# Kernel tuning notes

Hardware: AMD Instinct MI355X
Metric: run time of the kernel (lower is better)

Reference implementation:

```python
import jax, jax.numpy as jnp
import numpy as np

H = 16      # num_heads
D = 64      # head_dim
BQ = 64     # block_size_q
BKV = 64    # block_size_kv


def setup_inputs() -> dict:
    key = jax.random.key(0)
    ks = jax.random.split(key, 5)
    B, S, dim = 2, 2048, 1024
    x = jax.random.normal(ks[0], (B, S, dim), dtype=jnp.float32)
    Wq = jax.random.normal(ks[1], (dim, H * D), dtype=jnp.float32) * 0.02
    Wk = jax.random.normal(ks[2], (dim, H * D), dtype=jnp.float32) * 0.02
    Wv = jax.random.normal(ks[3], (dim, H * D), dtype=jnp.float32) * 0.02
    Wo = jax.random.normal(ks[4], (H * D, dim), dtype=jnp.float32) * 0.02
    return {"x": x, "Wq": Wq, "Wk": Wk, "Wv": Wv, "Wo": Wo}


def _flash_tiled(q, k, v, scale):
    # q,k,v: (B, H, S, D). Non-causal tiled attention with online softmax,
    # faithfully replicating the source's per-iteration division by l_new.
    B, nh, S, d = q.shape
    nq, nkv = S // BQ, S // BKV
    qb = q.reshape(B, nh, nq, BQ, d)                       # all q blocks at once (outer loop vectorized)
    kb = k.reshape(B, nh, nkv, BKV, d).transpose(2, 0, 1, 3, 4)  # (nkv, B, H, BKV, D)
    vb = v.reshape(B, nh, nkv, BKV, d).transpose(2, 0, 1, 3, 4)

    o0 = jnp.zeros((B, nh, nq, BQ, d), q.dtype)
    m0 = jnp.full((B, nh, nq, BQ), -jnp.inf, q.dtype)
    l0 = jnp.zeros((B, nh, nq, BQ), q.dtype)

    def step(carry, kv):
        o, m, l = carry
        kj, vj = kv
        s = jnp.einsum('bhnqd,bhkd->bhnqk', qb, kj) * scale   # (B,H,nq,BQ,BKV)
        m_new = jnp.maximum(m, s.max(axis=-1))
        p = jnp.exp(s - m_new[..., None])
        alpha = jnp.exp(m - m_new)
        l_new = alpha * l + p.sum(axis=-1)
        # NOTE: division by l_new every iteration, as in the source module.
        o_new = (alpha[..., None] * o + jnp.einsum('bhnqk,bhkd->bhnqd', p, vj)) / l_new[..., None]
        return (o_new, m_new, l_new), None

    (o, _, _), _ = jax.lax.scan(step, (o0, m0, l0), (kb, vb))
    return o.reshape(B, nh, S, d)


def reference(x, Wq, Wk, Wv, Wo):
    B, S, dim = x.shape
    scale = D ** -0.5
    q = (x @ Wq).reshape(B, S, H, D).transpose(0, 2, 1, 3)
    k = (x @ Wk).reshape(B, S, H, D).transpose(0, 2, 1, 3)
    v = (x @ Wv).reshape(B, S, H, D).transpose(0, 2, 1, 3)
    o = _flash_tiled(q, k, v, scale)                       # (B,H,S,D)
    out = o.transpose(0, 2, 1, 3).reshape(B, S, H * D)
    return out @ Wo
```

## Files before the change

### kernel.cpp

```cpp
#include <hip/hip_runtime.h>
#include <hip/hip_bf16.h>
#include <math.h>

#define BB   2
#define SS   2048
#define DIM  1024
#define NH   16
#define HD   64
#define MTOT (BB * SS)

typedef unsigned short ushortT;
typedef __attribute__((ext_vector_type(8))) short short8v;
typedef __attribute__((ext_vector_type(4))) float float4v;

union FragU { short8v v; unsigned short us[8]; unsigned int u[4]; };

__device__ inline unsigned short f2bf(float x) {
    unsigned u = __builtin_bit_cast(unsigned, x);
    u += 0x7fffu + ((u >> 16) & 1u);
    return (unsigned short)(u >> 16);
}
__device__ inline float bf2f(unsigned short h) {
    unsigned u = ((unsigned)h) << 16;
    return __builtin_bit_cast(float, u);
}
__device__ inline void split_tr(float x, unsigned short& hi, unsigned short& lo) {
    unsigned u = __builtin_bit_cast(unsigned, x);
    hi = (unsigned short)(u >> 16);
    float hf = __builtin_bit_cast(float, u & 0xffff0000u);
    lo = (unsigned short)(__builtin_bit_cast(unsigned, x - hf) >> 16);
}
__device__ inline void split4(const float4& x, short4& hi, short4& lo) {
    unsigned short h0 = f2bf(x.x), h1 = f2bf(x.y), h2 = f2bf(x.z), h3 = f2bf(x.w);
    hi = make_short4((short)h0, (short)h1, (short)h2, (short)h3);
    lo = make_short4((short)f2bf(x.x - bf2f(h0)), (short)f2bf(x.y - bf2f(h1)),
                     (short)f2bf(x.z - bf2f(h2)), (short)f2bf(x.w - bf2f(h3)));
}
__device__ inline void gld_lds16(const void* g, void* l) {
    __builtin_amdgcn_global_load_lds(
        (const __attribute__((address_space(1))) void*)g,
        (__attribute__((address_space(3))) void*)l, 16, 0, 0);
}

__global__ __launch_bounds__(256) void convert_split_kernel(
    const float* __restrict__ in, ushortT* __restrict__ hi, ushortT* __restrict__ lo, int n4)
{
    int t = blockIdx.x * 256 + threadIdx.x;
    if (t < n4) {
        float4 x = ((const float4*)in)[t];
        short4 h, l; split4(x, h, l);
        ((short4*)hi)[t] = h;
        ((short4*)lo)[t] = l;
    }
}

__global__ __launch_bounds__(256) void transpose_split_kernel(
    const float* __restrict__ W0, const float* __restrict__ W1,
    const float* __restrict__ W2, const float* __restrict__ W3,
    ushortT* __restrict__ WtH, ushortT* __restrict__ WtL)
{
    const int z = blockIdx.z;
    const float* __restrict__ W = (z == 0) ? W0 : (z == 1) ? W1 : (z == 2) ? W2 : W3;
    ushortT* H = WtH + (size_t)z * 1024 * 1024;
    ushortT* L = WtL + (size_t)z * 1024 * 1024;

    __shared__ float T[64][65];
    const int k0 = blockIdx.y * 64, n0 = blockIdx.x * 64;
    const int tid = threadIdx.x;
    const int c4 = (tid & 15) * 4;

#pragma unroll
    for (int i = 0; i < 4; i++) {
        int r = (tid >> 4) + 16 * i;
        *(float4*)&T[r][c4] = *(const float4*)(W + (size_t)(k0 + r) * 1024 + n0 + c4);
    }
    __syncthreads();
#pragma unroll
    for (int i = 0; i < 4; i++) {
        int n = (tid >> 4) + 16 * i;
        float4 vv = make_float4(T[c4 + 0][n], T[c4 + 1][n], T[c4 + 2][n], T[c4 + 3][n]);
        short4 h, l; split4(vv, h, l);
        *(short4*)&H[(size_t)(n0 + n) * 1024 + k0 + c4] = h;
        *(short4*)&L[(size_t)(n0 + n) * 1024 + k0 + c4] = l;
    }
}

__global__ __launch_bounds__(256) void kv_convert_kernel(
    const float* __restrict__ kw, const float* __restrict__ vw,
    ushortT* __restrict__ KhG, ushortT* __restrict__ KlG,
    ushortT* __restrict__ VhG, ushortT* __restrict__ VlG)
{
    const int which = blockIdx.z;
    const int jb = blockIdx.x, bh = blockIdx.y;
    const int b = bh >> 4, h = bh & 15;
    const float* __restrict__ in = which ? vw : kw;
    ushortT* __restrict__ OH = which ? VhG : KhG;
    ushortT* __restrict__ OL = which ? VlG : KlG;

    __shared__ float T[64][68];
    const int tid = threadIdx.x;
    const size_t ibase = (size_t)b * SS * DIM + (size_t)h * HD + (size_t)(jb * 64) * DIM;
    const int c4 = (tid & 15) * 4;
#pragma unroll
    for (int i = 0; i < 4; i++) {
        int r = (tid >> 4) + 16 * i;
        *(float4*)&T[r][c4] = *(const float4*)(in + ibase + (size_t)r * DIM + c4);
    }
    __syncthreads();

    ushortT* oh = OH + (size_t)(bh * 32 + jb) * 4096;
    ushortT* ol = OL + (size_t)(bh * 32 + jb) * 4096;

#pragma unroll
    for (int i = 0; i < 2; i++) {
        const int s = tid + i * 256;
        const int f = s >> 6;
        const int lane = s & 63;
        const int ks = f >> 2, c = f & 3;
        const int qd = lane >> 4, l15 = lane & 15;
        ushortT hv[8], lv[8];
        if (which == 0) {
            const int kv = c * 16 + l15;
            const int d0 = ks * 32 + qd * 8;
#pragma unroll
            for (int j = 0; j < 8; j++) split_tr(T[kv][d0 + j], hv[j], lv[j]);
        } else {
            const int d = c * 16 + l15;
            const int kv0 = ks * 32 + qd * 8;
#pragma unroll
            for (int j = 0; j < 8; j++) split_tr(T[kv0 + j][d], hv[j], lv[j]);
        }
        *(short4*)&oh[s * 8]     = *(short4*)&hv[0];
        *(short4*)&oh[s * 8 + 4] = *(short4*)&hv[4];
        *(short4*)&ol[s * 8]     = *(short4*)&lv[0];
        *(short4*)&ol[s * 8 + 4] = *(short4*)&lv[4];
    }
}

__global__ __launch_bounds__(256, 2) void gemm_bt_split_kernel(
    const ushortT* __restrict__ Ah, const ushortT* __restrict__ Al,
    const ushortT* __restrict__ BtH, const ushortT* __restrict__ BtL,
    float* __restrict__ Y0, float* __restrict__ Y1, float* __restrict__ Y2)
{
    const int z = blockIdx.z;
    const ushortT* __restrict__ Bh = BtH + (size_t)z * 1024 * 1024;
    const ushortT* __restrict__ Bl = BtL + (size_t)z * 1024 * 1024;
    float* __restrict__ Y = (z == 0) ? Y0 : (z == 1) ? Y1 : Y2;

    const int K = 1024, N = 1024;
    const int m0 = blockIdx.y * 128;
    const int n0 = blockIdx.x * 128;

    __shared__ __align__(16) ushortT AhS[128 * 32];
    __shared__ __align__(16) ushortT AlS[128 * 32];
    __shared__ __align__(16) ushortT BhS[128 * 32];
    __shared__ __align__(16) ushortT BlS[128 * 32];

    const int tid  = threadIdx.x;
    const int wave = tid >> 6, lane = tid & 63;
    const int quad = lane >> 4, l15 = lane & 15;
    const int wm = wave >> 1, wn = wave & 1;

    const int s0 = tid, s1 = tid + 256;
    const int ar0 = s0 >> 2, ak0 = (s0 & 3) * 8;
    const int ar1 = s1 >> 2, ak1 = (s1 & 3) * 8;

    float4v acc[4][4];
#pragma unroll
    for (int i = 0; i < 4; i++)
#pragma unroll
        for (int j = 0; j < 4; j++) acc[i][j] = (float4v){0.f, 0.f, 0.f, 0.f};

    for (int k0 = 0; k0 < K; k0 += 32) {
        __syncthreads();
        gld_lds16(Ah + (size_t)(m0 + ar0) * K + k0 + ak0, &AhS[s0 * 8]);
        gld_lds16(Ah + (size_t)(m0 + ar1) * K + k0 + ak1, &AhS[s1 * 8]);
        gld_lds16(Al + (size_t)(m0 + ar0) * K + k0 + ak0, &AlS[s0 * 8]);
        gld_lds16(Al + (size_t)(m0 + ar1) * K + k0 + ak1, &AlS[s1 * 8]);
        gld_lds16(Bh + (size_t)(n0 + ar0) * K + k0 + ak0, &BhS[s0 * 8]);
        gld_lds16(Bh + (size_t)(n0 + ar1) * K + k0 + ak1, &BhS[s1 * 8]);
        gld_lds16(Bl + (size_t)(n0 + ar0) * K + k0 + ak0, &BlS[s0 * 8]);
        gld_lds16(Bl + (size_t)(n0 + ar1) * K + k0 + ak1, &BlS[s1 * 8]);
        __syncthreads();

        FragU ah[4], al[4], bh[4], bl[4];
#pragma unroll
        for (int t = 0; t < 4; t++) {
            ah[t].v = *(const short8v*)&AhS[(wm * 64 + t * 16 + l15) * 32 + quad * 8];
            al[t].v = *(const short8v*)&AlS[(wm * 64 + t * 16 + l15) * 32 + quad * 8];
            bh[t].v = *(const short8v*)&BhS[(wn * 64 + t * 16 + l15) * 32 + quad * 8];
            bl[t].v = *(const short8v*)&BlS[(wn * 64 + t * 16 + l15) * 32 + quad * 8];
        }
#pragma unroll
        for (int mt = 0; mt < 4; mt++)
#pragma unroll
            for (int nt = 0; nt < 4; nt++) {
                acc[mt][nt] = __builtin_amdgcn_mfma_f32_16x16x32_bf16(ah[mt].v, bh[nt].v, acc[mt][nt], 0, 0, 0);
                acc[mt][nt] = __builtin_amdgcn_mfma_f32_16x16x32_bf16(ah[mt].v, bl[nt].v, acc[mt][nt], 0, 0, 0);
                acc[mt][nt] = __builtin_amdgcn_mfma_f32_16x16x32_bf16(al[mt].v, bh[nt].v, acc[mt][nt], 0, 0, 0);
            }
    }

#pragma unroll
    for (int mt = 0; mt < 4; mt++)
#pragma unroll
        for (int r = 0; r < 4; r++) {
            const int row = m0 + wm * 64 + mt * 16 + quad * 4 + r;
            float* yp = Y + (size_t)row * N + n0 + wn * 64 + l15;
#pragma unroll
            for (int nt = 0; nt < 4; nt++)
                yp[nt * 16] = acc[mt][nt][r];
        }
}

__global__ __launch_bounds__(256, 2) void attn_mfma_kernel(
    const float* __restrict__ q,
    const ushortT* __restrict__ KhG, const ushortT* __restrict__ KlG,
    const ushortT* __restrict__ VhG, const ushortT* __restrict__ VlG,
    ushortT* __restrict__ Oh, ushortT* __restrict__ Ol)
{
    __shared__ __align__(16) ushortT KhS[4096];
    __shared__ __align__(16) ushortT KlS[4096];
    __shared__ __align__(16) ushortT VhS[4096];
    __shared__ __align__(16) ushortT VlS[4096];
    __shared__ __align__(16) ushortT PW[4][2][2048];

    const int tid  = threadIdx.x;
    const int wave = tid >> 6, lane = tid & 63;
    const int quad = lane >> 4, l15 = lane & 15;
    const int bh = blockIdx.y, b = bh >> 4, h = bh & 15;
    const size_t base = (size_t)b * SS * DIM + (size_t)h * HD;
    const int qs0 = blockIdx.x * 128 + wave * 32;

    const float qscale = 0.125f * 1.4426950408889634f;
    FragU Qh[2][2], Ql[2][2];
#pragma unroll
    for (int rt = 0; rt < 2; rt++) {
        const int qrow = qs0 + rt * 16 + l15;
#pragma unroll
        for (int ks = 0; ks < 2; ks++) {
            const float* p0 = q + base + (size_t)qrow * DIM + ks * 32 + quad * 8;
            float4 a = *(const float4*)(p0);
            float4 c = *(const float4*)(p0 + 4);
            float e[8] = {a.x, a.y, a.z, a.w, c.x, c.y, c.z, c.w};
#pragma unroll
            for (int j = 0; j < 8; j++) {
                float x = e[j] * qscale;
                unsigned short hs = f2bf(x);
                Qh[rt][ks].us[j] = hs;
                Ql[rt][ks].us[j] = f2bf(x - bf2f(hs));
            }
        }
    }

    FragU onesF;
#pragma unroll
    for (int i = 0; i < 4; i++) onesF.u[i] = 0x3F803F80u;

    float4v Oacc[4][2];
#pragma unroll
    for (int dt = 0; dt < 4; dt++)
#pragma unroll
        for (int rt = 0; rt < 2; rt++) Oacc[dt][rt] = (float4v){0.f, 0.f, 0.f, 0.f};

    float m_run[2] = {-INFINITY, -INFINITY};
    float l_run[2] = {0.f, 0.f};

    const int sl0 = wave * 128 + lane, sl1 = sl0 + 64;
    ushortT* ph = &PW[wave][0][0];
    ushortT* pl = &PW[wave][1][0];
    const int pwq = ((quad >> 1) * 16 + l15) * 8 + (quad & 1) * 4;

    for (int jb = 0; jb < 32; jb++) {
        __syncthreads();
        {
            const size_t tb = (size_t)(bh * 32 + jb) * 4096;
            gld_lds16(KhG + tb + sl0 * 8, &KhS[sl0 * 8]);
            gld_lds16(KhG + tb + sl1 * 8, &KhS[sl1 * 8]);
            gld_lds16(KlG + tb + sl0 * 8, &KlS[sl0 * 8]);
            gld_lds16(KlG + tb + sl1 * 8, &KlS[sl1 * 8]);
            gld_lds16(VhG + tb + sl0 * 8, &VhS[sl0 * 8]);
            gld_lds16(VhG + tb + sl1 * 8, &VhS[sl1 * 8]);
            gld_lds16(VlG + tb + sl0 * 8, &VlS[sl0 * 8]);
            gld_lds16(VlG + tb + sl1 * 8, &VlS[sl1 * 8]);
        }
        __syncthreads();

        float4v st[4][2];
#pragma unroll
        for (int mt = 0; mt < 4; mt++)
#pragma unroll
            for (int rt = 0; rt < 2; rt++) st[mt][rt] = (float4v){0.f, 0.f, 0.f, 0.f};

#pragma unroll
        for (int ks = 0; ks < 2; ks++) {
            FragU kh[4], kl[4];
#pragma unroll
            for (int mt = 0; mt < 4; mt++) {
                kh[mt].v = *(const short8v*)&KhS[((ks * 4 + mt) * 64 + lane) * 8];
                kl[mt].v = *(const short8v*)&KlS[((ks * 4 + mt) * 64 + lane) * 8];
            }
#pragma unroll
            for (int mt = 0; mt < 4; mt++)
#pragma unroll
                for (int rt = 0; rt < 2; rt++) {
                    st[mt][rt] = __builtin_amdgcn_mfma_f32_16x16x32_bf16(kh[mt].v, Qh[rt][ks].v, st[mt][rt], 0, 0, 0);
                    st[mt][rt] = __builtin_amdgcn_mfma_f32_16x16x32_bf16(kh[mt].v, Ql[rt][ks].v, st[mt][rt], 0, 0, 0);
                    st[mt][rt] = __builtin_amdgcn_mfma_f32_16x16x32_bf16(kl[mt].v, Qh[rt][ks].v, st[mt][rt], 0, 0, 0);
                }
        }

        float mn[2], al[2];
#pragma unroll
        for (int rt = 0; rt < 2; rt++) {
            float v0 = fmaxf(fmaxf(st[0][rt][0], st[0][rt][1]), fmaxf(st[0][rt][2], st[0][rt][3]));
#pragma unroll
            for (int mt = 1; mt < 4; mt++) {
                float v1 = fmaxf(fmaxf(st[mt][rt][0], st[mt][rt][1]), fmaxf(st[mt][rt][2], st[mt][rt][3]));
                v0 = fmaxf(v0, v1);
            }
            v0 = fmaxf(v0, __shfl_xor(v0, 16, 64));
            v0 = fmaxf(v0, __shfl_xor(v0, 32, 64));
            mn[rt] = fmaxf(m_run[rt], v0);
            al[rt] = __builtin_amdgcn_exp2f(m_run[rt] - mn[rt]);
        }

#pragma unroll
        for (int mt = 0; mt < 4; mt++)
#pragma unroll
            for (int rt = 0; rt < 2; rt++)
#pragma unroll
                for (int r = 0; r < 4; r++)
                    st[mt][rt][r] = __builtin_amdgcn_exp2f(st[mt][rt][r] - mn[rt]);

#pragma unroll
        for (int rt = 0; rt < 2; rt++)
#pragma unroll
            for (int mt = 0; mt < 4; mt++) {
                unsigned u0 = __builtin_bit_cast(unsigned, st[mt][rt][0]);
                unsigned u1 = __builtin_bit_cast(unsigned, st[mt][rt][1]);
                unsigned u2 = __builtin_bit_cast(unsigned, st[mt][rt][2]);
                unsigned u3 = __builtin_bit_cast(unsigned, st[mt][rt][3]);
                unsigned h01 = (u0 >> 16) | (u1 & 0xffff0000u);
                unsigned h23 = (u2 >> 16) | (u3 & 0xffff0000u);
                float d0 = st[mt][rt][0] - __builtin_bit_cast(float, u0 & 0xffff0000u);
                float d1 = st[mt][rt][1] - __builtin_bit_cast(float, u1 & 0xffff0000u);
                float d2 = st[mt][rt][2] - __builtin_bit_cast(float, u2 & 0xffff0000u);
                float d3 = st[mt][rt][3] - __builtin_bit_cast(float, u3 & 0xffff0000u);
                unsigned l01 = (__builtin_bit_cast(unsigned, d0) >> 16) |
                               (__builtin_bit_cast(unsigned, d1) & 0xffff0000u);
                unsigned l23 = (__builtin_bit_cast(unsigned, d2) >> 16) |
                               (__builtin_bit_cast(unsigned, d3) & 0xffff0000u);
                const int idx = ((rt * 2 + (mt >> 1)) * 512 + (mt & 1) * 256) + pwq;
                *(uint2*)&ph[idx] = make_uint2(h01, h23);
                *(uint2*)&pl[idx] = make_uint2(l01, l23);
            }

        FragU Ph[2][2], Pl[2][2];
#pragma unroll
        for (int rt = 0; rt < 2; rt++)
#pragma unroll
            for (int ks = 0; ks < 2; ks++) {
                Ph[rt][ks].v = *(const short8v*)&ph[((rt * 2 + ks) * 64 + lane) * 8];
                Pl[rt][ks].v = *(const short8v*)&pl[((rt * 2 + ks) * 64 + lane) * 8];
            }

        float4v co[2];
        co[0] = (float4v){0.f, 0.f, 0.f, 0.f};
        co[1] = (float4v){0.f, 0.f, 0.f, 0.f};
#pragma unroll
        for (int rt = 0; rt < 2; rt++)
#pragma unroll
            for (int ks = 0; ks < 2; ks++) {
                co[rt] = __builtin_amdgcn_mfma_f32_16x16x32_bf16(onesF.v, Ph[rt][ks].v, co[rt], 0, 0, 0);
                co[rt] = __builtin_amdgcn_mfma_f32_16x16x32_bf16(onesF.v, Pl[rt][ks].v, co[rt], 0, 0, 0);
            }

        float ln[2];
#pragma unroll
        for (int rt = 0; rt < 2; rt++)
            ln[rt] = al[rt] * l_run[rt] + co[rt][0];

#pragma unroll
        for (int dt = 0; dt < 4; dt++)
#pragma unroll
            for (int rt = 0; rt < 2; rt++)
#pragma unroll
                for (int r = 0; r < 4; r++)
                    Oacc[dt][rt][r] *= al[rt];

#pragma unroll
        for (int ks = 0; ks < 2; ks++)
#pragma unroll
            for (int dt = 0; dt < 4; dt++) {
                FragU vh, vl;
                vh.v = *(const short8v*)&VhS[((ks * 4 + dt) * 64 + lane) * 8];
                vl.v = *(const short8v*)&VlS[((ks * 4 + dt) * 64 + lane) * 8];
#pragma unroll
                for (int rt = 0; rt < 2; rt++) {
                    Oacc[dt][rt] = __builtin_amdgcn_mfma_f32_16x16x32_bf16(vh.v, Ph[rt][ks].v, Oacc[dt][rt], 0, 0, 0);
                    Oacc[dt][rt] = __builtin_amdgcn_mfma_f32_16x16x32_bf16(vl.v, Ph[rt][ks].v, Oacc[dt][rt], 0, 0, 0);
                    Oacc[dt][rt] = __builtin_amdgcn_mfma_f32_16x16x32_bf16(vh.v, Pl[rt][ks].v, Oacc[dt][rt], 0, 0, 0);
                }
            }

#pragma unroll
        for (int rt = 0; rt < 2; rt++) {
            float inv = __builtin_amdgcn_rcpf(ln[rt]);
#pragma unroll
            for (int dt = 0; dt < 4; dt++)
#pragma unroll
                for (int r = 0; r < 4; r++)
                    Oacc[dt][rt][r] *= inv;
            m_run[rt] = mn[rt];
            l_run[rt] = ln[rt];
        }
    }

    float* Pf = (float*)&PW[wave][0][0];
    const int q16 = lane >> 2, c = lane & 3;
#pragma unroll
    for (int rt = 0; rt < 2; rt++) {
#pragma unroll
        for (int dt = 0; dt < 4; dt++)
            *(float4v*)&Pf[l15 * 68 + dt * 16 + quad * 4] = Oacc[dt][rt];
        float vals[16];
#pragma unroll
        for (int kk = 0; kk < 4; kk++)
            *(float4v*)&vals[kk * 4] = *(const float4v*)&Pf[q16 * 68 + c * 16 + kk * 4];

        unsigned ho[8], lo8[8];
#pragma unroll
        for (int kk = 0; kk < 8; kk++) {
            unsigned short h0, l0, h1, l1;
            split_tr(vals[2 * kk], h0, l0);
            split_tr(vals[2 * kk + 1], h1, l1);
            ho[kk]  = (unsigned)h0 | ((unsigned)h1 << 16);
            lo8[kk] = (unsigned)l0 | ((unsigned)l1 << 16);
        }
        const int qrow = qs0 + rt * 16 + q16;
        const size_t off = (size_t)(b * SS + qrow) * DIM + h * HD + c * 16;
        *(uint4*)&Oh[off]     = make_uint4(ho[0], ho[1], ho[2], ho[3]);
        *(uint4*)&Oh[off + 8] = make_uint4(ho[4], ho[5], ho[6], ho[7]);
        *(uint4*)&Ol[off]     = make_uint4(lo8[0], lo8[1], lo8[2], lo8[3]);
        *(uint4*)&Ol[off + 8] = make_uint4(lo8[4], lo8[5], lo8[6], lo8[7]);
    }
}

extern "C" void kernel_launch(void* const* d_in, const int* in_sizes, int n_in,
                              void* d_out, int out_size, void* d_ws, size_t ws_size,
                              hipStream_t stream)
{
    const float* x  = (const float*)d_in[0];
    const float* Wq = (const float*)d_in[1];
    const float* Wk = (const float*)d_in[2];
    const float* Wv = (const float*)d_in[3];
    const float* Wo = (const float*)d_in[4];
    float* out = (float*)d_out;

    char* w = (char*)d_ws;
    float*   qw  = (float*)(w);
    float*   kw  = (float*)(w + ((size_t)16 << 20));
    float*   vw  = (float*)(w + ((size_t)32 << 20));
    ushortT* XhS = (ushortT*)(w + ((size_t)48 << 20));
    ushortT* XlS = (ushortT*)(w + ((size_t)56 << 20));
    ushortT* WtH = (ushortT*)(w + ((size_t)64 << 20));
    ushortT* WtL = (ushortT*)(w + ((size_t)72 << 20));
    ushortT* KhG = (ushortT*)(w + ((size_t)80 << 20));
    ushortT* KlG = (ushortT*)(w + ((size_t)88 << 20));
    ushortT* VhG = XhS;
    ushortT* VlG = XlS;
    ushortT* OhS = (ushortT*)kw;
    ushortT* OlS = (ushortT*)(w + ((size_t)24 << 20));

    dim3 blk(256);
    const int n4 = MTOT * DIM / 4;

    convert_split_kernel<<<dim3(n4 / 256), blk, 0, stream>>>(x, XhS, XlS, n4);
    transpose_split_kernel<<<dim3(16, 16, 4), blk, 0, stream>>>(Wq, Wk, Wv, Wo, WtH, WtL);

    gemm_bt_split_kernel<<<dim3(8, 32, 3), blk, 0, stream>>>(XhS, XlS, WtH, WtL, qw, kw, vw);

    kv_convert_kernel<<<dim3(32, 32, 2), blk, 0, stream>>>(kw, vw, KhG, KlG, VhG, VlG);

    attn_mfma_kernel<<<dim3(16, 32), blk, 0, stream>>>(qw, KhG, KlG, VhG, VlG, OhS, OlS);

    gemm_bt_split_kernel<<<dim3(8, 32, 1), blk, 0, stream>>>(
        OhS, OlS, WtH + (size_t)3 * 1024 * 1024, WtL + (size_t)3 * 1024 * 1024,
        out, out, out);
}
```

Measured before the change: 337.6 us.

## Load K/V fragments directly from global, fold softmax normalisation into P

The attention kernel stops staging K and V tiles through shared memory with block-wide barriers. Each wave now loads its MFMA fragments straight from global memory, relying on the pre-packed fragment layout and cache reuse across the four waves. The row sum is computed with shuffles instead of a ones-vector MFMA, and P is pre-scaled by 1/l so the output rescale becomes one multiply. The GEMM launch bound is raised to 3 blocks per CU. The trade-off is more global/L2 traffic per wave and more live registers, and the changed rounding of the scaled P may shift precision slightly.

```diff
diff --git a/kernel.cpp b/kernel.cpp
--- a/kernel.cpp
+++ b/kernel.cpp
@@ -137,7 +137,7 @@
     }
 }
 
-__global__ __launch_bounds__(256, 2) void gemm_bt_split_kernel(
+__global__ __launch_bounds__(256, 3) void gemm_bt_split_kernel(
     const ushortT* __restrict__ Ah, const ushortT* __restrict__ Al,
     const ushortT* __restrict__ BtH, const ushortT* __restrict__ BtL,
     float* __restrict__ Y0, float* __restrict__ Y1, float* __restrict__ Y2)
@@ -219,10 +219,6 @@
     const ushortT* __restrict__ VhG, const ushortT* __restrict__ VlG,
     ushortT* __restrict__ Oh, ushortT* __restrict__ Ol)
 {
-    __shared__ __align__(16) ushortT KhS[4096];
-    __shared__ __align__(16) ushortT KlS[4096];
-    __shared__ __align__(16) ushortT VhS[4096];
-    __shared__ __align__(16) ushortT VlS[4096];
     __shared__ __align__(16) ushortT PW[4][2][2048];
 
     const int tid  = threadIdx.x;
@@ -253,10 +249,6 @@
         }
     }
 
-    FragU onesF;
-#pragma unroll
-    for (int i = 0; i < 4; i++) onesF.u[i] = 0x3F803F80u;
-
     float4v Oacc[4][2];
 #pragma unroll
     for (int dt = 0; dt < 4; dt++)
@@ -266,25 +258,22 @@
     float m_run[2] = {-INFINITY, -INFINITY};
     float l_run[2] = {0.f, 0.f};
 
-    const int sl0 = wave * 128 + lane, sl1 = sl0 + 64;
     ushortT* ph = &PW[wave][0][0];
     ushortT* pl = &PW[wave][1][0];
     const int pwq = ((quad >> 1) * 16 + l15) * 8 + (quad & 1) * 4;
+    const int lane8 = lane * 8;
 
     for (int jb = 0; jb < 32; jb++) {
-        __syncthreads();
-        {
-            const size_t tb = (size_t)(bh * 32 + jb) * 4096;
-            gld_lds16(KhG + tb + sl0 * 8, &KhS[sl0 * 8]);
-            gld_lds16(KhG + tb + sl1 * 8, &KhS[sl1 * 8]);
-            gld_lds16(KlG + tb + sl0 * 8, &KlS[sl0 * 8]);
-            gld_lds16(KlG + tb + sl1 * 8, &KlS[sl1 * 8]);
-            gld_lds16(VhG + tb + sl0 * 8, &VhS[sl0 * 8]);
-            gld_lds16(VhG + tb + sl1 * 8, &VhS[sl1 * 8]);
-            gld_lds16(VlG + tb + sl0 * 8, &VlS[sl0 * 8]);
-            gld_lds16(VlG + tb + sl1 * 8, &VlS[sl1 * 8]);
-        }
-        __syncthreads();
+        const size_t tb = (size_t)(bh * 32 + jb) * 4096;
+
+        FragU kh[2][4], kl[2][4];
+#pragma unroll
+        for (int ks = 0; ks < 2; ks++)
+#pragma unroll
+            for (int mt = 0; mt < 4; mt++) {
+                kh[ks][mt].v = *(const short8v*)&KhG[tb + ((ks * 4 + mt) * 64) * 8 + lane8];
+                kl[ks][mt].v = *(const short8v*)&KlG[tb + ((ks * 4 + mt) * 64) * 8 + lane8];
+            }
 
         float4v st[4][2];
 #pragma unroll
@@ -293,24 +282,17 @@
             for (int rt = 0; rt < 2; rt++) st[mt][rt] = (float4v){0.f, 0.f, 0.f, 0.f};
 
 #pragma unroll
-        for (int ks = 0; ks < 2; ks++) {
-            FragU kh[4], kl[4];
-#pragma unroll
-            for (int mt = 0; mt < 4; mt++) {
-                kh[mt].v = *(const short8v*)&KhS[((ks * 4 + mt) * 64 + lane) * 8];
-                kl[mt].v = *(const short8v*)&KlS[((ks * 4 + mt) * 64 + lane) * 8];
-            }
+        for (int ks = 0; ks < 2; ks++)
 #pragma unroll
             for (int mt = 0; mt < 4; mt++)
 #pragma unroll
                 for (int rt = 0; rt < 2; rt++) {
-                    st[mt][rt] = __builtin_amdgcn_mfma_f32_16x16x32_bf16(kh[mt].v, Qh[rt][ks].v, st[mt][rt], 0, 0, 0);
-                    st[mt][rt] = __builtin_amdgcn_mfma_f32_16x16x32_bf16(kh[mt].v, Ql[rt][ks].v, st[mt][rt], 0, 0, 0);
-                    st[mt][rt] = __builtin_amdgcn_mfma_f32_16x16x32_bf16(kl[mt].v, Qh[rt][ks].v, st[mt][rt], 0, 0, 0);
+                    st[mt][rt] = __builtin_amdgcn_mfma_f32_16x16x32_bf16(kh[ks][mt].v, Qh[rt][ks].v, st[mt][rt], 0, 0, 0);
+                    st[mt][rt] = __builtin_amdgcn_mfma_f32_16x16x32_bf16(kh[ks][mt].v, Ql[rt][ks].v, st[mt][rt], 0, 0, 0);
+                    st[mt][rt] = __builtin_amdgcn_mfma_f32_16x16x32_bf16(kl[ks][mt].v, Qh[rt][ks].v, st[mt][rt], 0, 0, 0);
                 }
-        }
-
-        float mn[2], al[2];
+
+        float oscale[2];
 #pragma unroll
         for (int rt = 0; rt < 2; rt++) {
             float v0 = fmaxf(fmaxf(st[0][rt][0], st[0][rt][1]), fmaxf(st[0][rt][2], st[0][rt][3]));
@@ -321,17 +303,31 @@
             }
             v0 = fmaxf(v0, __shfl_xor(v0, 16, 64));
             v0 = fmaxf(v0, __shfl_xor(v0, 32, 64));
-            mn[rt] = fmaxf(m_run[rt], v0);
-            al[rt] = __builtin_amdgcn_exp2f(m_run[rt] - mn[rt]);
-        }
-
-#pragma unroll
-        for (int mt = 0; mt < 4; mt++)
-#pragma unroll
-            for (int rt = 0; rt < 2; rt++)
+            const float mn = fmaxf(m_run[rt], v0);
+            const float al = __builtin_amdgcn_exp2f(m_run[rt] - mn);
+
+            float ssum = 0.f;
+#pragma unroll
+            for (int mt = 0; mt < 4; mt++)
+#pragma unroll
+                for (int r = 0; r < 4; r++) {
+                    const float p = __builtin_amdgcn_exp2f(st[mt][rt][r] - mn);
+                    st[mt][rt][r] = p;
+                    ssum += p;
+                }
+            ssum += __shfl_xor(ssum, 16, 64);
+            ssum += __shfl_xor(ssum, 32, 64);
+            const float ln = al * l_run[rt] + ssum;
+            const float inv = __builtin_amdgcn_rcpf(ln);
+            oscale[rt] = al * inv;
+#pragma unroll
+            for (int mt = 0; mt < 4; mt++)
 #pragma unroll
                 for (int r = 0; r < 4; r++)
-                    st[mt][rt][r] = __builtin_amdgcn_exp2f(st[mt][rt][r] - mn[rt]);
+                    st[mt][rt][r] *= inv;
+            m_run[rt] = mn;
+            l_run[rt] = ln;
+        }
 
 #pragma unroll
         for (int rt = 0; rt < 2; rt++)
@@ -356,30 +352,23 @@
                 *(uint2*)&pl[idx] = make_uint2(l01, l23);
             }
 
+        FragU vh[2][4], vl[2][4];
+#pragma unroll
+        for (int ks = 0; ks < 2; ks++)
+#pragma unroll
+            for (int dt = 0; dt < 4; dt++) {
+                vh[ks][dt].v = *(const short8v*)&VhG[tb + ((ks * 4 + dt) * 64) * 8 + lane8];
+                vl[ks][dt].v = *(const short8v*)&VlG[tb + ((ks * 4 + dt) * 64) * 8 + lane8];
+            }
+
         FragU Ph[2][2], Pl[2][2];
 #pragma unroll
         for (int rt = 0; rt < 2; rt++)
 #pragma unroll
             for (int ks = 0; ks < 2; ks++) {
-                Ph[rt][ks].v = *(const short8v*)&ph[((rt * 2 + ks) * 64 + lane) * 8];
-                Pl[rt][ks].v = *(const short8v*)&pl[((rt * 2 + ks) * 64 + lane) * 8];
-            }
-
-        float4v co[2];
-        co[0] = (float4v){0.f, 0.f, 0.f, 0.f};
-        co[1] = (float4v){0.f, 0.f, 0.f, 0.f};
-#pragma unroll
-        for (int rt = 0; rt < 2; rt++)
-#pragma unroll
-            for (int ks = 0; ks < 2; ks++) {
-                co[rt] = __builtin_amdgcn_mfma_f32_16x16x32_bf16(onesF.v, Ph[rt][ks].v, co[rt], 0, 0, 0);
-                co[rt] = __builtin_amdgcn_mfma_f32_16x16x32_bf16(onesF.v, Pl[rt][ks].v, co[rt], 0, 0, 0);
-            }
-
-        float ln[2];
-#pragma unroll
-        for (int rt = 0; rt < 2; rt++)
-            ln[rt] = al[rt] * l_run[rt] + co[rt][0];
+                Ph[rt][ks].v = *(const short8v*)&ph[((rt * 2 + ks) * 64) * 8 + lane8];
+                Pl[rt][ks].v = *(const short8v*)&pl[((rt * 2 + ks) * 64) * 8 + lane8];
+            }
 
 #pragma unroll
         for (int dt = 0; dt < 4; dt++)
@@ -387,34 +376,18 @@
             for (int rt = 0; rt < 2; rt++)
 #pragma unroll
                 for (int r = 0; r < 4; r++)
-                    Oacc[dt][rt][r] *= al[rt];
+                    Oacc[dt][rt][r] *= oscale[rt];
 
 #pragma unroll
         for (int ks = 0; ks < 2; ks++)
 #pragma unroll
-            for (int dt = 0; dt < 4; dt++) {
-                FragU vh, vl;
-                vh.v = *(const short8v*)&VhS[((ks * 4 + dt) * 64 + lane) * 8];
-                vl.v = *(const short8v*)&VlS[((ks * 4 + dt) * 64 + lane) * 8];
+            for (int dt = 0; dt < 4; dt++)
 #pragma unroll
                 for (int rt = 0; rt < 2; rt++) {
-                    Oacc[dt][rt] = __builtin_amdgcn_mfma_f32_16x16x32_bf16(vh.v, Ph[rt][ks].v, Oacc[dt][rt], 0, 0, 0);
-                    Oacc[dt][rt] = __builtin_amdgcn_mfma_f32_16x16x32_bf16(vl.v, Ph[rt][ks].v, Oacc[dt][rt], 0, 0, 0);
-                    Oacc[dt][rt] = __builtin_amdgcn_mfma_f32_16x16x32_bf16(vh.v, Pl[rt][ks].v, Oacc[dt][rt], 0, 0, 0);
+                    Oacc[dt][rt] = __builtin_amdgcn_mfma_f32_16x16x32_bf16(vh[ks][dt].v, Ph[rt][ks].v, Oacc[dt][rt], 0, 0, 0);
+                    Oacc[dt][rt] = __builtin_amdgcn_mfma_f32_16x16x32_bf16(vl[ks][dt].v, Ph[rt][ks].v, Oacc[dt][rt], 0, 0, 0);
+                    Oacc[dt][rt] = __builtin_amdgcn_mfma_f32_16x16x32_bf16(vh[ks][dt].v, Pl[rt][ks].v, Oacc[dt][rt], 0, 0, 0);
                 }
-            }
-
-#pragma unroll
-        for (int rt = 0; rt < 2; rt++) {
-            float inv = __builtin_amdgcn_rcpf(ln[rt]);
-#pragma unroll
-            for (int dt = 0; dt < 4; dt++)
-#pragma unroll
-                for (int r = 0; r < 4; r++)
-                    Oacc[dt][rt][r] *= inv;
-            m_run[rt] = mn[rt];
-            l_run[rt] = ln[rt];
-        }
     }
 
     float* Pf = (float*)&PW[wave][0][0];
```

Result: slower. 367.5 us (+8.9%).
